# Kernel tuning notes

Measured on AMD Instinct MI355X. Metric: run time of the kernel, lower is better.

## Reference

```python
import jax, jax.numpy as jnp
import numpy as np

B, S = 64, 512
VOCAB, DIM, FFDIM, NHEADS, BLOCKS = 512, 128, 512, 4, 4
MASK_INTER_CHOICES = False
LN_EPS = 1e-5
NEG = -1e30


def setup_inputs() -> dict:
    key = jax.random.key(0)
    ks = jax.random.split(key, 12)
    s = 0.02
    inp = dict(
        token_idxes=jax.random.randint(ks[0], (B, S), 0, VOCAB),
        n_pad_lefts=jax.random.randint(ks[1], (B,), 0, 9),
        cards_picked_n=jax.random.randint(ks[2], (B,), 1, 4),
        cards_skipped_n=jax.random.randint(ks[3], (B,), 1, 4),
        n_upgrades=jax.random.randint(ks[4], (B, S), 0, 3),
        emb=jax.random.normal(ks[5], (VOCAB, DIM), jnp.float32) * s,
        in_proj_w=jax.random.normal(ks[6], (BLOCKS, 3 * DIM, DIM), jnp.float32) * s,
        in_proj_b=jnp.zeros((BLOCKS, 3 * DIM), jnp.float32),
        out_w=jax.random.normal(ks[7], (BLOCKS, DIM, DIM), jnp.float32) * s,
        out_b=jnp.zeros((BLOCKS, DIM), jnp.float32),
        ln1_g=jnp.ones((BLOCKS, DIM), jnp.float32),
        ln1_b=jnp.zeros((BLOCKS, DIM), jnp.float32),
        ff1_w=jax.random.normal(ks[8], (BLOCKS, FFDIM, DIM), jnp.float32) * s,
        ff1_b=jnp.zeros((BLOCKS, FFDIM), jnp.float32),
        ff2_w=jax.random.normal(ks[9], (BLOCKS, DIM, FFDIM), jnp.float32) * s,
        ff2_b=jnp.zeros((BLOCKS, DIM), jnp.float32),
        ln2_g=jnp.ones((BLOCKS, DIM), jnp.float32),
        ln2_b=jnp.zeros((BLOCKS, DIM), jnp.float32),
        proj_w=jax.random.normal(ks[10], (2, DIM), jnp.float32) * s,
        proj_b=jnp.zeros((2,), jnp.float32),
    )
    return inp


def build_allowed(n_pad, n_choice):
    # allowed[b, i, j] == True where attention is permitted (torch mask==0)
    pos = jnp.arange(S)
    i = pos[None, :, None]
    j = pos[None, None, :]
    npd = n_pad[:, None, None]
    nc = n_choice[:, None, None]
    mid_i = (i >= npd) & (i < S - nc)
    mid_j = (j >= npd) & (j < S - nc)
    ch_i = i >= S - nc
    ch_j = j >= S - nc
    allowed = ((i < npd) & (i == j)) | (mid_i & mid_j) | (ch_i & mid_j)
    if MASK_INTER_CHOICES:
        allowed = allowed | (ch_i & (i == j))
    else:
        allowed = allowed | (ch_i & ch_j)
    return allowed  # [B, S, S]


def layernorm(x, g, b):
    m = jnp.mean(x, axis=-1, keepdims=True)
    v = jnp.var(x, axis=-1, keepdims=True)
    return (x - m) / jnp.sqrt(v + LN_EPS) * g + b


def mha_block(x, allowed, w_in, b_in, w_out, b_out, g1, b1, w1, bf1, w2, bf2, g2, b2):
    hd = DIM // NHEADS
    qkv = x @ w_in.T + b_in                       # [B,S,3D]
    q, k, v = jnp.split(qkv, 3, axis=-1)
    def heads(t):
        return t.reshape(x.shape[0], S, NHEADS, hd).transpose(0, 2, 1, 3)
    q, k, v = heads(q), heads(k), heads(v)
    scores = jnp.einsum('bhqd,bhkd->bhqk', q, k) / np.float32(np.sqrt(hd))
    scores = jnp.where(allowed[:, None, :, :], scores, NEG)
    attn = jax.nn.softmax(scores, axis=-1)
    o = jnp.einsum('bhqk,bhkd->bhqd', attn, v)
    o = o.transpose(0, 2, 1, 3).reshape(x.shape[0], S, DIM)
    o = o @ w_out.T + b_out
    x = layernorm(x + o, g1, b1)
    ff = jax.nn.relu(x @ w1.T + bf1) @ w2.T + bf2
    return layernorm(x + ff, g2, b2)


def reference(token_idxes, n_pad_lefts, cards_picked_n, cards_skipped_n, n_upgrades,
              emb, in_proj_w, in_proj_b, out_w, out_b, ln1_g, ln1_b,
              ff1_w, ff1_b, ff2_w, ff2_b, ln2_g, ln2_b, proj_w, proj_b):
    n_choice = cards_picked_n + cards_skipped_n
    feat = emb[token_idxes]                                   # [B,S,D]
    pos = jnp.arange(S)
    ch0 = (pos[None, :] >= n_choice[:, None]).astype(feat.dtype)
    feat = feat.at[:, :, 0].set(ch0)
    feat = feat.at[:, :, 1].set(jnp.clip(n_upgrades, 0, 1).astype(feat.dtype))
    allowed = build_allowed(n_pad_lefts, n_choice)
    for l in range(BLOCKS):
        feat = mha_block(feat, allowed, in_proj_w[l], in_proj_b[l], out_w[l], out_b[l],
                         ln1_g[l], ln1_b[l], ff1_w[l], ff1_b[l], ff2_w[l], ff2_b[l],
                         ln2_g[l], ln2_b[l])
    logits = feat @ proj_w.T + proj_b                          # [B,S,2]
    return jax.nn.softmax(logits, axis=2)
```

## Files before the change

kernel.cpp:

```cpp
#include <hip/hip_runtime.h>

#define CB   64
#define CS   512
#define CD   128
#define CH   4
#define CFF  512
#define CL   4
#define NEG_BIG -3.0e38f
#define SCALE 0.17677669529663687f
#define EXSC  0.25505654050961364f

typedef __attribute__((ext_vector_type(8))) short short8;
typedef __attribute__((ext_vector_type(4))) float f32x4;
typedef __attribute__((ext_vector_type(4))) unsigned int u32x4;

static __device__ __forceinline__ unsigned short f2b(float f) {
  union { float f; unsigned int u; } v; v.f = f;
  unsigned int u = v.u;
  unsigned int r = (u + 0x7fffu + ((u >> 16) & 1u)) >> 16;
  return (unsigned short)r;
}

__global__ void k_cvt_all(const float* __restrict__ inw, const float* __restrict__ outw,
                          const float* __restrict__ ffw1, const float* __restrict__ ffw2,
                          unsigned short* __restrict__ wq, unsigned short* __restrict__ wo,
                          unsigned short* __restrict__ w1, unsigned short* __restrict__ w2) {
  int bid = blockIdx.x;
  if (bid < 512) {
    const float* src; unsigned short* dst; int base;
    if (bid < 192)      { src = inw;  dst = wq; base = bid; }
    else if (bid < 256) { src = outw; dst = wo; base = bid - 192; }
    else                { src = ffw1; dst = w1; base = bid - 256; }
    int i = base * 256 + threadIdx.x;
    float4 v = ((const float4*)src)[i];
    ((ushort4*)dst)[i] = make_ushort4(f2b(v.x), f2b(v.y), f2b(v.z), f2b(v.w));
  } else {
    int i = (bid - 512) * 256 + threadIdx.x;
    int flat = i * 4;
    int row = flat >> 9;
    int n = flat & 511;
    float4 v = ((const float4*)ffw2)[i];
    int pos = (n & 480) + 8 * ((n & 15) >> 2) + 4 * ((n >> 4) & 1);
    *(ushort4*)&w2[(size_t)row * 512 + pos] =
        make_ushort4(f2b(v.x), f2b(v.y), f2b(v.z), f2b(v.w));
  }
}

__global__ void k_embed(const int* __restrict__ tok, const int* __restrict__ picked,
                        const int* __restrict__ skipped, const int* __restrict__ nupg,
                        const float* __restrict__ emb, float* __restrict__ featf,
                        unsigned short* __restrict__ featb) {
  int idx = blockIdx.x * 256 + threadIdx.x;
  int tp = idx >> 5, c4 = idx & 31;
  int t = tok[tp];
  float4 v = ((const float4*)emb)[t * 32 + c4];
  if (c4 == 0) {
    int b = tp >> 9, s = tp & 511;
    int nc = picked[b] + skipped[b];
    v.x = (s >= nc) ? 1.f : 0.f;
    v.y = (nupg[tp] > 0) ? 1.f : 0.f;
  }
  ((float4*)featf)[idx] = v;
  ((ushort4*)featb)[idx] = make_ushort4(f2b(v.x), f2b(v.y), f2b(v.z), f2b(v.w));
}

__global__ __launch_bounds__(256, 2) void k_gemm_qkv(
    const unsigned short* __restrict__ A, const unsigned short* __restrict__ W,
    const float* __restrict__ bias, unsigned short* __restrict__ qb,
    unsigned short* __restrict__ kb, unsigned short* __restrict__ vtb) {
  const int tid = threadIdx.x;
  const int m0 = blockIdx.x * 128;
  const int y = blockIdx.y;
  const int n0 = y * 128;
  const int lane = tid & 63, wid = tid >> 6;
  const int wm = wid >> 1, wn = wid & 1;
  const int lg = lane >> 4, r = lane & 15;

  f32x4 acc[4][4];
#pragma unroll
  for (int mi = 0; mi < 4; ++mi)
#pragma unroll
    for (int ni = 0; ni < 4; ++ni) acc[mi][ni] = (f32x4){0.f, 0.f, 0.f, 0.f};

  const unsigned short* Ab = A + (size_t)(m0 + wm * 64 + r) * 128 + lg * 8;
  const unsigned short* Wb = W + (size_t)(n0 + wn * 64 + r) * 128 + lg * 8;
#pragma unroll
  for (int kc = 0; kc < 4; ++kc) {
    short8 af[4], wf[4];
#pragma unroll
    for (int mi = 0; mi < 4; ++mi) af[mi] = *(const short8*)(Ab + mi * 2048 + kc * 32);
#pragma unroll
    for (int ni = 0; ni < 4; ++ni) wf[ni] = *(const short8*)(Wb + ni * 2048 + kc * 32);
#pragma unroll
    for (int mi = 0; mi < 4; ++mi)
#pragma unroll
      for (int ni = 0; ni < 4; ++ni)
        acc[mi][ni] = __builtin_amdgcn_mfma_f32_16x16x32_bf16(
            af[mi], wf[ni], acc[mi][ni], 0, 0, 0);
  }

  const int bidx = m0 >> 9;
  if (y < 2) {
    unsigned short* dst = y ? kb : qb;
    const float sc = y ? 1.f : EXSC;
#pragma unroll
    for (int mi = 0; mi < 4; ++mi)
#pragma unroll
      for (int ni = 0; ni < 4; ++ni) {
        int cl = wn * 64 + ni * 16 + r;
        int h = cl >> 5, dd = cl & 31;
        float bia = bias[n0 + cl];
        unsigned short* dp =
            dst + ((size_t)(bidx * 4 + h) * 512) * 32 + dd;
#pragma unroll
        for (int reg = 0; reg < 4; ++reg) {
          int s = (m0 + wm * 64 + mi * 16 + 4 * lg + reg) & 511;
          dp[(size_t)s * 32] = f2b((acc[mi][ni][reg] + bia) * sc);
        }
      }
  } else {
#pragma unroll
    for (int mi = 0; mi < 4; ++mi)
#pragma unroll
      for (int ni = 0; ni < 4; ++ni) {
        int cl = wn * 64 + ni * 16 + r;
        int h = cl >> 5, dd = cl & 31;
        float bia = bias[256 + cl];
        int s4 = (m0 + wm * 64 + mi * 16 + 4 * lg) & 511;
        int chunk = s4 >> 5, jl = s4 & 31;
        int p = 8 * ((jl & 15) >> 2) + 4 * (jl >> 4);
        ushort4 pk = make_ushort4(
            f2b(acc[mi][ni][0] + bia), f2b(acc[mi][ni][1] + bia),
            f2b(acc[mi][ni][2] + bia), f2b(acc[mi][ni][3] + bia));
        *(ushort4*)&vtb[((size_t)(bidx * 4 + h) * 32 + dd) * 512 + chunk * 32 + p] = pk;
      }
  }
}

__global__ __launch_bounds__(512, 1) void k_attn2(
    const unsigned short* __restrict__ qb, const unsigned short* __restrict__ kb,
    const unsigned short* __restrict__ vtb, const int* __restrict__ npadp,
    const int* __restrict__ picked, const int* __restrict__ skipped,
    unsigned short* __restrict__ obufb) {
  __shared__ __align__(16) unsigned short Ks[CS * 40];
  __shared__ __align__(16) unsigned short Vt[32 * CS];
  const int bh = blockIdx.x, b = bh >> 2, h = bh & 3;
  const int tid = threadIdx.x;
  const unsigned short* qbp = qb + ((size_t)bh * 512) * 32;
  const unsigned short* kbp = kb + ((size_t)bh * 512) * 32;
  const unsigned short* vtp = vtb + ((size_t)bh * 32) * 512;
#pragma unroll
  for (int i = 0; i < 4; ++i) {
    int f = tid + i * 512;
    int row = f >> 2, c = f & 3;
    *(uint4*)&Ks[row * 40 + c * 8] = *(const uint4*)(kbp + row * 32 + c * 8);
    int rowd = f >> 6, c16 = f & 63;
    *(uint4*)((char*)Vt + rowd * 1024 + ((c16 * 16) ^ ((rowd & 7) << 4))) =
        *(const uint4*)(vtp + rowd * 512 + c16 * 8);
  }
  const int lane = tid & 63, w = tid >> 6;
  const int lg = lane >> 4, r = lane & 15;
  const int npd = npadp[b];
  const int jhi_mid = CS - (picked[b] + skipped[b]);
  short8 onesf;
#pragma unroll
  for (int e = 0; e < 8; ++e) onesf[e] = (short)0x3F80;
  __syncthreads();

  short8 qf[4];
  int jhiR[4];
#pragma unroll
  for (int qt = 0; qt < 4; ++qt) {
    int q = w * 64 + qt * 16 + r;
    qf[qt] = *(const short8*)(qbp + (size_t)q * 32 + 8 * lg);
    jhiR[qt] = (q < jhi_mid) ? jhi_mid : CS;
  }
  f32x4 aO0[4], aO1[4], aL[4];
#pragma unroll
  for (int qt = 0; qt < 4; ++qt) {
    aO0[qt] = (f32x4){0.f, 0.f, 0.f, 0.f};
    aO1[qt] = (f32x4){0.f, 0.f, 0.f, 0.f};
    aL[qt]  = (f32x4){0.f, 0.f, 0.f, 0.f};
  }

  for (int jc = 0; jc < 16; ++jc) {
    const int j0 = jc * 32;
    short8 kf0 = *(const short8*)&Ks[(j0 + r) * 40 + 8 * lg];
    short8 kf1 = *(const short8*)&Ks[(j0 + 16 + r) * 40 + 8 * lg];
    const int jby = (j0 * 2 + 16 * lg) ^ ((r & 7) << 4);
    short8 vf0 = *(const short8*)((const char*)Vt + r * 1024 + jby);
    short8 vf1 = *(const short8*)((const char*)Vt + (16 + r) * 1024 + jby);
#pragma unroll
    for (int qt = 0; qt < 4; ++qt) {
      f32x4 z = (f32x4){0.f, 0.f, 0.f, 0.f};
      f32x4 s0 = __builtin_amdgcn_mfma_f32_16x16x32_bf16(kf0, qf[qt], z, 0, 0, 0);
      f32x4 s1 = __builtin_amdgcn_mfma_f32_16x16x32_bf16(kf1, qf[qt], z, 0, 0, 0);
      float p0[4], p1[4];
#pragma unroll
      for (int g = 0; g < 4; ++g) {
        p0[g] = exp2f(fminf(s0[g], 43.f));
        p1[g] = exp2f(fminf(s1[g], 43.f));
      }
      if (jc == 0) {
#pragma unroll
        for (int g = 0; g < 4; ++g)
          p0[g] = (4 * lg + g >= npd) ? p0[g] : 0.f;
      }
      if (jc == 15) {
#pragma unroll
        for (int g = 0; g < 4; ++g)
          p1[g] = (496 + 4 * lg + g < jhiR[qt]) ? p1[g] : 0.f;
      }
      unsigned int d0 = ((unsigned int)f2b(p0[1]) << 16) | f2b(p0[0]);
      unsigned int d1 = ((unsigned int)f2b(p0[3]) << 16) | f2b(p0[2]);
      unsigned int d2 = ((unsigned int)f2b(p1[1]) << 16) | f2b(p1[0]);
      unsigned int d3 = ((unsigned int)f2b(p1[3]) << 16) | f2b(p1[2]);
      u32x4 pd = (u32x4){d0, d1, d2, d3};
      short8 pa = __builtin_bit_cast(short8, pd);
      aL[qt]  = __builtin_amdgcn_mfma_f32_16x16x32_bf16(pa, onesf, aL[qt], 0, 0, 0);
      aO0[qt] = __builtin_amdgcn_mfma_f32_16x16x32_bf16(pa, vf0, aO0[qt], 0, 0, 0);
      aO1[qt] = __builtin_amdgcn_mfma_f32_16x16x32_bf16(pa, vf1, aO1[qt], 0, 0, 0);
    }
  }

#pragma unroll
  for (int qt = 0; qt < 4; ++qt)
#pragma unroll
    for (int g = 0; g < 4; ++g) {
      int qg = w * 64 + qt * 16 + 4 * lg + g;
      float inv = 1.f / aL[qt][g];
      unsigned short o0 = f2b(aO0[qt][g] * inv);
      unsigned short o1 = f2b(aO1[qt][g] * inv);
      if (qg < npd) {
        int p = 8 * (qg >> 2) + (qg & 3);
        o0 = *(const unsigned short*)((const char*)Vt + r * 1024 +
                                      ((2 * p) ^ ((r & 7) << 4)));
        o1 = *(const unsigned short*)((const char*)Vt + (16 + r) * 1024 +
                                      ((2 * p) ^ ((r & 7) << 4)));
      }
      unsigned short* op = obufb + ((size_t)(b * 512 + qg)) * 128 + h * 32;
      op[r] = o0;
      op[16 + r] = o1;
    }
}

__global__ __launch_bounds__(256, 2) void k_gemm_ln(
    const unsigned short* __restrict__ A, const unsigned short* __restrict__ W,
    const float* __restrict__ bias, float* __restrict__ outf,
    unsigned short* __restrict__ outb, const float* __restrict__ resf,
    const float* __restrict__ gam, const float* __restrict__ bet) {
  const int tid = threadIdx.x;
  const int m0 = blockIdx.x * 128;
  const int lane = tid & 63, wid = tid >> 6;
  const int wm = wid >> 1, wn = wid & 1;
  const int lg = lane >> 4, r = lane & 15;

  f32x4 acc[4][4];
#pragma unroll
  for (int mi = 0; mi < 4; ++mi)
#pragma unroll
    for (int ni = 0; ni < 4; ++ni) acc[mi][ni] = (f32x4){0.f, 0.f, 0.f, 0.f};

  const unsigned short* Ab = A + (size_t)(m0 + wm * 64 + r) * 128 + lg * 8;
  const unsigned short* Wb = W + (size_t)(wn * 64 + r) * 128 + lg * 8;
#pragma unroll
  for (int kc = 0; kc < 4; ++kc) {
    short8 af[4], wf[4];
#pragma unroll
    for (int mi = 0; mi < 4; ++mi) af[mi] = *(const short8*)(Ab + mi * 2048 + kc * 32);
#pragma unroll
    for (int ni = 0; ni < 4; ++ni) wf[ni] = *(const short8*)(Wb + ni * 2048 + kc * 32);
#pragma unroll
    for (int mi = 0; mi < 4; ++mi)
#pragma unroll
      for (int ni = 0; ni < 4; ++ni)
        acc[mi][ni] = __builtin_amdgcn_mfma_f32_16x16x32_bf16(
            af[mi], wf[ni], acc[mi][ni], 0, 0, 0);
  }

  __shared__ __align__(16) float Y[128 * 132];
#pragma unroll
  for (int mi = 0; mi < 4; ++mi)
#pragma unroll
    for (int ni = 0; ni < 4; ++ni) {
      int col = wn * 64 + ni * 16 + r;
      float bia = bias[col];
#pragma unroll
      for (int reg = 0; reg < 4; ++reg) {
        int row = wm * 64 + mi * 16 + 4 * lg + reg;
        Y[row * 132 + col] =
            acc[mi][ni][reg] + bia + resf[(size_t)(m0 + row) * 128 + col];
      }
    }
  __syncthreads();
  const int rr = tid >> 1, qq = tid & 1;
  float sum = 0.f, sum2 = 0.f;
  float4 yv[16];
#pragma unroll
  for (int c = 0; c < 16; ++c) {
    float4 y = *(const float4*)&Y[rr * 132 + qq * 64 + c * 4];
    yv[c] = y;
    sum += y.x + y.y + y.z + y.w;
    sum2 += y.x * y.x + y.y * y.y + y.z * y.z + y.w * y.w;
  }
  sum += __shfl_xor(sum, 1);
  sum2 += __shfl_xor(sum2, 1);
  const float mean = sum * (1.f / 128.f);
  const float var = sum2 * (1.f / 128.f) - mean * mean;
  const float rstd = rsqrtf(var + 1e-5f);
#pragma unroll
  for (int c = 0; c < 16; ++c) {
    float4 gv = ((const float4*)gam)[qq * 16 + c];
    float4 bv = ((const float4*)bet)[qq * 16 + c];
    float4 y = yv[c];
    y.x = (y.x - mean) * rstd * gv.x + bv.x;
    y.y = (y.y - mean) * rstd * gv.y + bv.y;
    y.z = (y.z - mean) * rstd * gv.z + bv.z;
    y.w = (y.w - mean) * rstd * gv.w + bv.w;
    ((float4*)outf)[(size_t)(m0 + rr) * 32 + qq * 16 + c] = y;
    *(ushort4*)&outb[(size_t)(m0 + rr) * 128 + qq * 64 + c * 4] =
        make_ushort4(f2b(y.x), f2b(y.y), f2b(y.z), f2b(y.w));
  }
}

__global__ __launch_bounds__(256, 2) void k_ffn2(
    const unsigned short* __restrict__ x, const unsigned short* __restrict__ w1b,
    const float* __restrict__ b1, const unsigned short* __restrict__ w2p,
    const float* __restrict__ b2, const float* __restrict__ gam,
    const float* __restrict__ bet, float* __restrict__ featf,
    unsigned short* __restrict__ featb) {
  const int tid = threadIdx.x;
  const int lane = tid & 63, w = tid >> 6;
  const int lg = lane >> 4, r = lane & 15;
  const int tokb = blockIdx.x * 64 + w * 16;

  short8 xf[4];
  const unsigned short* xp = x + (size_t)(tokb + r) * 128 + lg * 8;
#pragma unroll
  for (int kc = 0; kc < 4; ++kc) xf[kc] = *(const short8*)(xp + kc * 32);

  f32x4 aO[8];
#pragma unroll
  for (int dt = 0; dt < 8; ++dt) aO[dt] = (f32x4){0.f, 0.f, 0.f, 0.f};

  const unsigned short* w1base = w1b + (size_t)r * 128 + lg * 8;
  const unsigned short* w2base = w2p + (size_t)r * 512 + lg * 8;

#pragma unroll
  for (int c = 0; c < 16; ++c) {
    f32x4 hA = (f32x4){0.f, 0.f, 0.f, 0.f};
    f32x4 hB = (f32x4){0.f, 0.f, 0.f, 0.f};
#pragma unroll
    for (int kc = 0; kc < 4; ++kc) {
      short8 wA = *(const short8*)(w1base + (size_t)(32 * c) * 128 + kc * 32);
      short8 wB = *(const short8*)(w1base + (size_t)(32 * c + 16) * 128 + kc * 32);
      hA = __builtin_amdgcn_mfma_f32_16x16x32_bf16(wA, xf[kc], hA, 0, 0, 0);
      hB = __builtin_amdgcn_mfma_f32_16x16x32_bf16(wB, xf[kc], hB, 0, 0, 0);
    }
    float pA[4], pB[4];
#pragma unroll
    for (int g = 0; g < 4; ++g) {
      pA[g] = fmaxf(hA[g] + b1[32 * c + 4 * lg + g], 0.f);
      pB[g] = fmaxf(hB[g] + b1[32 * c + 16 + 4 * lg + g], 0.f);
    }
    unsigned int d0 = ((unsigned int)f2b(pA[1]) << 16) | f2b(pA[0]);
    unsigned int d1 = ((unsigned int)f2b(pA[3]) << 16) | f2b(pA[2]);
    unsigned int d2 = ((unsigned int)f2b(pB[1]) << 16) | f2b(pB[0]);
    unsigned int d3 = ((unsigned int)f2b(pB[3]) << 16) | f2b(pB[2]);
    u32x4 pd = (u32x4){d0, d1, d2, d3};
    short8 pa = __builtin_bit_cast(short8, pd);
#pragma unroll
    for (int dt = 0; dt < 8; ++dt) {
      short8 w2f = *(const short8*)(w2base + (size_t)(dt * 16) * 512 + c * 32);
      aO[dt] = __builtin_amdgcn_mfma_f32_16x16x32_bf16(pa, w2f, aO[dt], 0, 0, 0);
    }
  }

  float b2v[8], gv[8], bv[8];
#pragma unroll
  for (int dt = 0; dt < 8; ++dt) {
    b2v[dt] = b2[r + 16 * dt];
    gv[dt]  = gam[r + 16 * dt];
    bv[dt]  = bet[r + 16 * dt];
  }
  float yv[8][4];
  float s1[4] = {0.f, 0.f, 0.f, 0.f}, s2[4] = {0.f, 0.f, 0.f, 0.f};
#pragma unroll
  for (int g = 0; g < 4; ++g) {
    const float* fp = featf + (size_t)(tokb + 4 * lg + g) * 128 + r;
#pragma unroll
    for (int dt = 0; dt < 8; ++dt) {
      float t = aO[dt][g] + b2v[dt] + fp[16 * dt];
      yv[dt][g] = t;
      s1[g] += t;
      s2[g] += t * t;
    }
  }
#pragma unroll
  for (int g = 0; g < 4; ++g) {
#pragma unroll
    for (int d = 1; d < 16; d <<= 1) {
      s1[g] += __shfl_xor(s1[g], d);
      s2[g] += __shfl_xor(s2[g], d);
    }
    const float mean = s1[g] * (1.f / 128.f);
    const float var = s2[g] * (1.f / 128.f) - mean * mean;
    const float rstd = rsqrtf(var + 1e-5f);
    float* fo = featf + (size_t)(tokb + 4 * lg + g) * 128 + r;
    unsigned short* bo = featb + (size_t)(tokb + 4 * lg + g) * 128 + r;
#pragma unroll
    for (int dt = 0; dt < 8; ++dt) {
      float yy = (yv[dt][g] - mean) * rstd * gv[dt] + bv[dt];
      fo[16 * dt] = yy;
      bo[16 * dt] = f2b(yy);
    }
  }
}

__global__ void k_final(const float* __restrict__ feat, const float* __restrict__ pw,
                        const float* __restrict__ pb, float* __restrict__ out) {
  const int tid = threadIdx.x;
  const int tokb = blockIdx.x * 64 + (tid >> 2);
  const int qq = tid & 3;
  float d0 = 0.f, d1 = 0.f;
#pragma unroll
  for (int c = 0; c < 8; ++c) {
    float4 xv = ((const float4*)feat)[tokb * 32 + qq * 8 + c];
    float4 w0 = ((const float4*)pw)[qq * 8 + c];
    float4 w1 = ((const float4*)pw)[32 + qq * 8 + c];
    d0 += xv.x * w0.x + xv.y * w0.y + xv.z * w0.z + xv.w * w0.w;
    d1 += xv.x * w1.x + xv.y * w1.y + xv.z * w1.z + xv.w * w1.w;
  }
  d0 += __shfl_xor(d0, 1); d0 += __shfl_xor(d0, 2);
  d1 += __shfl_xor(d1, 1); d1 += __shfl_xor(d1, 2);
  if (qq == 0) {
    float l0 = d0 + pb[0], l1 = d1 + pb[1];
    float mx = fmaxf(l0, l1);
    float e0 = __expf(l0 - mx), e1 = __expf(l1 - mx);
    float inv = 1.f / (e0 + e1);
    ((float2*)out)[tokb] = make_float2(e0 * inv, e1 * inv);
  }
}

extern "C" void kernel_launch(void* const* d_in, const int* in_sizes, int n_in,
                              void* d_out, int out_size, void* d_ws, size_t ws_size,
                              hipStream_t stream) {
  const int* tok     = (const int*)d_in[0];
  const int* npad    = (const int*)d_in[1];
  const int* picked  = (const int*)d_in[2];
  const int* skipped = (const int*)d_in[3];
  const int* nupg    = (const int*)d_in[4];
  const float* emb   = (const float*)d_in[5];
  const float* inw   = (const float*)d_in[6];
  const float* inb   = (const float*)d_in[7];
  const float* outw  = (const float*)d_in[8];
  const float* outb_ = (const float*)d_in[9];
  const float* g1    = (const float*)d_in[10];
  const float* b1    = (const float*)d_in[11];
  const float* ffw1  = (const float*)d_in[12];
  const float* ffb1  = (const float*)d_in[13];
  const float* ffw2  = (const float*)d_in[14];
  const float* ffb2  = (const float*)d_in[15];
  const float* g2    = (const float*)d_in[16];
  const float* b2    = (const float*)d_in[17];
  const float* pw    = (const float*)d_in[18];
  const float* pb    = (const float*)d_in[19];

  char* wsb = (char*)d_ws;
  float*          featf = (float*)(wsb);
  unsigned short* qb    = (unsigned short*)(wsb + 16777216);
  unsigned short* kbuf  = (unsigned short*)(wsb + 25165824);
  unsigned short* vtb   = (unsigned short*)(wsb + 33554432);
  unsigned short* featb = (unsigned short*)(wsb + 41943040);
  unsigned short* obufb = (unsigned short*)(wsb + 50331648);
  unsigned short* wqkvb = (unsigned short*)(wsb + 58720256);
  unsigned short* woutb = (unsigned short*)(wsb + 59113472);
  unsigned short* wff1b = (unsigned short*)(wsb + 59244544);
  unsigned short* wff2p = (unsigned short*)(wsb + 59768832);

  k_cvt_all<<<dim3(768), 256, 0, stream>>>(inw, outw, ffw1, ffw2,
                                           wqkvb, woutb, wff1b, wff2p);

  k_embed<<<dim3(CB * CS * 32 / 256), 256, 0, stream>>>(
      tok, picked, skipped, nupg, emb, featf, featb);

  for (int l = 0; l < CL; ++l) {
    k_gemm_qkv<<<dim3(256, 3), 256, 0, stream>>>(
        featb, wqkvb + (size_t)l * 49152, inb + (size_t)l * 384, qb, kbuf, vtb);
    k_attn2<<<dim3(CB * CH), 512, 0, stream>>>(
        qb, kbuf, vtb, npad, picked, skipped, obufb);
    k_gemm_ln<<<dim3(256), 256, 0, stream>>>(
        obufb, woutb + (size_t)l * 16384, outb_ + (size_t)l * 128,
        featf, featb, featf, g1 + (size_t)l * 128, b1 + (size_t)l * 128);
    k_ffn2<<<dim3(512), 256, 0, stream>>>(
        featb, wff1b + (size_t)l * 65536, ffb1 + (size_t)l * 512,
        wff2p + (size_t)l * 65536, ffb2 + (size_t)l * 128,
        g2 + (size_t)l * 128, b2 + (size_t)l * 128, featf, featb);
  }

  k_final<<<dim3(CB * CS / 64), 256, 0, stream>>>(featf, pw, pb, (float*)d_out);
}
```

Baseline: 684.0 us.

## Stage FFN weights through double-buffered swizzled LDS instead of direct global loads

```diff
diff --git a/kernel.cpp b/kernel.cpp
--- a/kernel.cpp
+++ b/kernel.cpp
@@ -323,12 +323,13 @@
   }
 }
 
-__global__ __launch_bounds__(256, 2) void k_ffn2(
+__global__ __launch_bounds__(256, 2) void k_ffn3(
     const unsigned short* __restrict__ x, const unsigned short* __restrict__ w1b,
     const float* __restrict__ b1, const unsigned short* __restrict__ w2p,
     const float* __restrict__ b2, const float* __restrict__ gam,
     const float* __restrict__ bet, float* __restrict__ featf,
     unsigned short* __restrict__ featb) {
+  __shared__ __align__(16) char lds[65536];
   const int tid = threadIdx.x;
   const int lane = tid & 63, w = tid >> 6;
   const int lg = lane >> 4, r = lane & 15;
@@ -343,36 +344,86 @@
 #pragma unroll
   for (int dt = 0; dt < 8; ++dt) aO[dt] = (f32x4){0.f, 0.f, 0.f, 0.f};
 
-  const unsigned short* w1base = w1b + (size_t)r * 128 + lg * 8;
-  const unsigned short* w2base = w2p + (size_t)r * 512 + lg * 8;
-
-#pragma unroll
-  for (int c = 0; c < 16; ++c) {
-    f32x4 hA = (f32x4){0.f, 0.f, 0.f, 0.f};
-    f32x4 hB = (f32x4){0.f, 0.f, 0.f, 0.f};
+  const int f1row[4] = {(tid) >> 4, (tid + 256) >> 4, (tid + 512) >> 4, (tid + 768) >> 4};
+  const int f1c[4]   = {tid & 15, tid & 15, tid & 15, tid & 15};
+  const int f2row[4] = {(tid) >> 3, (tid + 256) >> 3, (tid + 512) >> 3, (tid + 768) >> 3};
+  const int f2c[4]   = {tid & 7, tid & 7, tid & 7, tid & 7};
+
+  uint4 pre1[4], pre2[4];
+#pragma unroll
+  for (int t = 0; t < 4; ++t) {
+    pre1[t] = *(const uint4*)(w1b + (size_t)f1row[t] * 128 + f1c[t] * 8);
+    pre2[t] = *(const uint4*)(w2p + (size_t)f2row[t] * 512 + f2c[t] * 8);
+  }
+#pragma unroll
+  for (int t = 0; t < 4; ++t) {
+    *(uint4*)(lds + f1row[t] * 256 + ((f1c[t] * 16) ^ ((f1row[t] & 7) << 4))) = pre1[t];
+    *(uint4*)(lds + 32768 + f2row[t] * 128 + ((f2c[t] * 16) ^ ((f2row[t] & 7) << 4))) = pre2[t];
+  }
+
+#pragma unroll
+  for (int c = 0; c < 8; ++c) {
+    if (c < 7) {
+#pragma unroll
+      for (int t = 0; t < 4; ++t) {
+        pre1[t] = *(const uint4*)(w1b + (size_t)((c + 1) * 64 + f1row[t]) * 128 + f1c[t] * 8);
+        pre2[t] = *(const uint4*)(w2p + (size_t)f2row[t] * 512 + (c + 1) * 64 + f2c[t] * 8);
+      }
+    }
+    __syncthreads();
+    const char* W1L = lds + (c & 1) * 16384;
+    const char* W2L = lds + 32768 + (c & 1) * 16384;
+
+    f32x4 hf[4];
+#pragma unroll
+    for (int nf = 0; nf < 4; ++nf) hf[nf] = (f32x4){0.f, 0.f, 0.f, 0.f};
 #pragma unroll
     for (int kc = 0; kc < 4; ++kc) {
-      short8 wA = *(const short8*)(w1base + (size_t)(32 * c) * 128 + kc * 32);
-      short8 wB = *(const short8*)(w1base + (size_t)(32 * c + 16) * 128 + kc * 32);
-      hA = __builtin_amdgcn_mfma_f32_16x16x32_bf16(wA, xf[kc], hA, 0, 0, 0);
-      hB = __builtin_amdgcn_mfma_f32_16x16x32_bf16(wB, xf[kc], hB, 0, 0, 0);
-    }
-    float pA[4], pB[4];
-#pragma unroll
-    for (int g = 0; g < 4; ++g) {
-      pA[g] = fmaxf(hA[g] + b1[32 * c + 4 * lg + g], 0.f);
-      pB[g] = fmaxf(hB[g] + b1[32 * c + 16 + 4 * lg + g], 0.f);
-    }
-    unsigned int d0 = ((unsigned int)f2b(pA[1]) << 16) | f2b(pA[0]);
-    unsigned int d1 = ((unsigned int)f2b(pA[3]) << 16) | f2b(pA[2]);
-    unsigned int d2 = ((unsigned int)f2b(pB[1]) << 16) | f2b(pB[0]);
-    unsigned int d3 = ((unsigned int)f2b(pB[3]) << 16) | f2b(pB[2]);
-    u32x4 pd = (u32x4){d0, d1, d2, d3};
-    short8 pa = __builtin_bit_cast(short8, pd);
+#pragma unroll
+      for (int nf = 0; nf < 4; ++nf) {
+        short8 wfr = *(const short8*)(W1L + (16 * nf + r) * 256 +
+                                      ((kc * 64 + lg * 16) ^ ((r & 7) << 4)));
+        hf[nf] = __builtin_amdgcn_mfma_f32_16x16x32_bf16(wfr, xf[kc], hf[nf], 0, 0, 0);
+      }
+    }
+    const float* b1c = b1 + 64 * c;
+    float pv[4][4];
+#pragma unroll
+    for (int nf = 0; nf < 4; ++nf)
+#pragma unroll
+      for (int g = 0; g < 4; ++g)
+        pv[nf][g] = fmaxf(hf[nf][g] + b1c[16 * nf + 4 * lg + g], 0.f);
+    unsigned int e0 = ((unsigned int)f2b(pv[0][1]) << 16) | f2b(pv[0][0]);
+    unsigned int e1 = ((unsigned int)f2b(pv[0][3]) << 16) | f2b(pv[0][2]);
+    unsigned int e2 = ((unsigned int)f2b(pv[1][1]) << 16) | f2b(pv[1][0]);
+    unsigned int e3 = ((unsigned int)f2b(pv[1][3]) << 16) | f2b(pv[1][2]);
+    unsigned int e4 = ((unsigned int)f2b(pv[2][1]) << 16) | f2b(pv[2][0]);
+    unsigned int e5 = ((unsigned int)f2b(pv[2][3]) << 16) | f2b(pv[2][2]);
+    unsigned int e6 = ((unsigned int)f2b(pv[3][1]) << 16) | f2b(pv[3][0]);
+    unsigned int e7 = ((unsigned int)f2b(pv[3][3]) << 16) | f2b(pv[3][2]);
+    u32x4 pd0 = (u32x4){e0, e1, e2, e3};
+    u32x4 pd1 = (u32x4){e4, e5, e6, e7};
+    short8 pa0 = __builtin_bit_cast(short8, pd0);
+    short8 pa1 = __builtin_bit_cast(short8, pd1);
+
 #pragma unroll
     for (int dt = 0; dt < 8; ++dt) {
-      short8 w2f = *(const short8*)(w2base + (size_t)(dt * 16) * 512 + c * 32);
-      aO[dt] = __builtin_amdgcn_mfma_f32_16x16x32_bf16(pa, w2f, aO[dt], 0, 0, 0);
+      short8 w2f0 = *(const short8*)(W2L + (16 * dt + r) * 128 +
+                                     ((lg * 16) ^ ((r & 7) << 4)));
+      short8 w2f1 = *(const short8*)(W2L + (16 * dt + r) * 128 +
+                                     ((64 + lg * 16) ^ ((r & 7) << 4)));
+      aO[dt] = __builtin_amdgcn_mfma_f32_16x16x32_bf16(pa0, w2f0, aO[dt], 0, 0, 0);
+      aO[dt] = __builtin_amdgcn_mfma_f32_16x16x32_bf16(pa1, w2f1, aO[dt], 0, 0, 0);
+    }
+
+    if (c < 7) {
+      char* W1N = lds + ((c + 1) & 1) * 16384;
+      char* W2N = lds + 32768 + ((c + 1) & 1) * 16384;
+#pragma unroll
+      for (int t = 0; t < 4; ++t) {
+        *(uint4*)(W1N + f1row[t] * 256 + ((f1c[t] * 16) ^ ((f1row[t] & 7) << 4))) = pre1[t];
+        *(uint4*)(W2N + f2row[t] * 128 + ((f2c[t] * 16) ^ ((f2row[t] & 7) << 4))) = pre2[t];
+      }
     }
   }
 
@@ -492,7 +543,7 @@
     k_gemm_ln<<<dim3(256), 256, 0, stream>>>(
         obufb, woutb + (size_t)l * 16384, outb_ + (size_t)l * 128,
         featf, featb, featf, g1 + (size_t)l * 128, b1 + (size_t)l * 128);
-    k_ffn2<<<dim3(512), 256, 0, stream>>>(
+    k_ffn3<<<dim3(512), 256, 0, stream>>>(
         featb, wff1b + (size_t)l * 65536, ffb1 + (size_t)l * 512,
         wff2p + (size_t)l * 65536, ffb2 + (size_t)l * 128,
         g2 + (size_t)l * 128, b2 + (size_t)l * 128, featf, featb);
```

Result: faster. 621.5 us (-9.1%).
